# Kernel tuning notes

Measured on AMD Instinct MI355X. Metric: run time of the kernel, lower is better.

## Reference

```python
import jax, jax.numpy as jnp
import numpy as np

# Module config (init_kwargs): nodes = (64, 64)
NX, NY_NODES = 64, 64


def setup_inputs() -> dict:
    key = jax.random.key(0)
    data = jax.random.normal(key, (4, 3, 1024, 1024), dtype=jnp.float32)
    return {"data": data}


def reference(data):
    B, C, H, W = data.shape
    scale = W // NX                    # = 16
    ny = H // scale                    # grid rows (= 64 here)
    nx = NX
    N = nx * ny                        # num_nodes = 4096
    p = scale - 1                      # original slices x1:x2 with x2=x1+scale-1 -> (scale-1) pixels

    # [B, C, ny, p, nx, p] top-left (scale-1)x(scale-1) sub-patch of each grid cell
    patches = data.reshape(B, C, ny, scale, nx, scale)[:, :, :, :p, :, :p]

    # L1 affinity between vertically / horizontally adjacent patches
    dv = jnp.abs(patches[:, :, 1:] - patches[:, :, :-1]).sum(axis=(1, 3, 5))          # [B, ny-1, nx]
    dh = jnp.abs(patches[:, :, :, :, 1:] - patches[:, :, :, :, :-1]).sum(axis=(1, 3, 5))  # [B, ny, nx-1]

    node = jnp.arange(ny)[:, None] * nx + jnp.arange(nx)[None, :]  # node_id = x + y*nx

    A = jnp.zeros((B, N, N), dtype=data.dtype)
    # vertical edges: self<->up/down
    lo_v = node[1:, :].ravel()   # lower cell of each vertical pair
    hi_v = node[:-1, :].ravel()  # upper cell
    dv_f = dv.reshape(B, -1)
    A = A.at[:, lo_v, hi_v].set(dv_f)   # self -> up
    A = A.at[:, hi_v, lo_v].set(dv_f)   # self -> down
    # horizontal edges: self<->left/right
    le_h = node[:, :-1].ravel()
    ri_h = node[:, 1:].ravel()
    dh_f = dh.reshape(B, -1)
    A = A.at[:, le_h, ri_h].set(dh_f)   # self -> right
    A = A.at[:, ri_h, le_h].set(dh_f)   # self -> left

    return A, data
```

## Files before the change

### kernel.cpp

```cpp
#include <hip/hip_runtime.h>

#define BB 4
#define CC 3
#define HH 1024
#define WW 1024
#define NXG 64
#define NYG 64
#define SCALE 16
#define PP 15
#define NNODE 4096

static const long long A_ELEMS    = (long long)BB * NNODE * NNODE;
static const long long DATA_ELEMS = (long long)BB * CC * HH * WW;

#define NV_PER_B 4032
#define NH_PER_B 4032
#define NV_TOT   16128
#define NE_TOT   32256

#define COPY_BLOCKS 512
#define EDGE_BLOCKS 8064

__global__ __launch_bounds__(256) void edge_copy_scatter(const float* __restrict__ data,
                                                         float* __restrict__ out) {
    if (blockIdx.x < COPY_BLOCKS) {
        long long i = (long long)blockIdx.x * 256 + threadIdx.x;
        const long long stride = (long long)COPY_BLOCKS * 256;
        const float4* __restrict__ src = (const float4*)data;
        float4* __restrict__ dst = (float4*)(out + A_ELEMS);
        const long long nvec = DATA_ELEMS / 4;
        for (; i < nvec; i += stride) dst[i] = src[i];
        return;
    }

    const int wave = (blockIdx.x - COPY_BLOCKS) * 4 + (threadIdx.x >> 6);
    const int lane = threadIdx.x & 63;
    const int r = lane >> 2;
    const int q = lane & 3;

    int b, y, x, n_lo, n_hi;
    long long delta;
    if (wave < NV_TOT) {
        const int e = wave;
        b = e / NV_PER_B; const int rem = e - b * NV_PER_B;
        y = rem >> 6; x = rem & 63;
        delta = (long long)SCALE * WW;
        n_lo = y * NXG + x; n_hi = n_lo + NXG;
    } else {
        const int e = wave - NV_TOT;
        b = e / NH_PER_B; const int rem = e - b * NH_PER_B;
        y = rem / 63; x = rem - y * 63;
        delta = SCALE;
        n_lo = y * NXG + x; n_hi = n_lo + 1;
    }

    const float* p0 = data + (((long long)(b * CC)) * HH + (long long)y * SCALE + r) * WW
                           + x * SCALE + q * 4;
    float s = 0.f;
    if (r < PP) {
        #pragma unroll
        for (int c = 0; c < CC; ++c) {
            const float* p = p0 + (long long)c * HH * WW;
            const float4 a  = *(const float4*)p;
            const float4 nb = *(const float4*)(p + delta);
            float d = fabsf(nb.x - a.x) + fabsf(nb.y - a.y) + fabsf(nb.z - a.z);
            if (q != 3) d += fabsf(nb.w - a.w);
            s += d;
        }
    }
    #pragma unroll
    for (int off = 32; off; off >>= 1) s += __shfl_down(s, off, 64);

    if (lane == 0) {
        float* Ab = out + (long long)b * NNODE * NNODE;
        Ab[(long long)n_hi * NNODE + n_lo] = s;
        Ab[(long long)n_lo * NNODE + n_hi] = s;
    }
}

extern "C" void kernel_launch(void* const* d_in, const int* in_sizes, int n_in,
                              void* d_out, int out_size, void* d_ws, size_t ws_size,
                              hipStream_t stream) {
    const float* data = (const float*)d_in[0];
    float* out = (float*)d_out;

    hipMemsetAsync(out, 0, (size_t)A_ELEMS * sizeof(float), stream);

    edge_copy_scatter<<<COPY_BLOCKS + EDGE_BLOCKS, 256, 0, stream>>>(data, out);
}
```

Measured before the change: 355.3 us.

## Fuse zero-fill with edge scatter by writing full adjacency rows per node

Removes the separate memset of the 256 MB adjacency matrix. Each node now gets one block that computes its four neighbour affinities and writes its whole output row, zeros included, with nontemporal vector stores. The data copy also switches to nontemporal stores. Each edge affinity is now computed twice, once from each endpoint, and a block barrier is added. The total output written stays the same, but it now happens in a single kernel with one pass of stores.

```diff
diff --git a/kernel.cpp b/kernel.cpp
--- a/kernel.cpp
+++ b/kernel.cpp
@@ -5,64 +5,61 @@
 #define HH 1024
 #define WW 1024
 #define NXG 64
-#define NYG 64
 #define SCALE 16
 #define PP 15
 #define NNODE 4096
 
+typedef float floatx4 __attribute__((ext_vector_type(4)));
+
 static const long long A_ELEMS    = (long long)BB * NNODE * NNODE;
 static const long long DATA_ELEMS = (long long)BB * CC * HH * WW;
 
-#define NV_PER_B 4032
-#define NH_PER_B 4032
-#define NV_TOT   16128
-#define NE_TOT   32256
+#define COPY_BLOCKS 512
+#define ROW_BLOCKS  (BB * NNODE)
 
-#define COPY_BLOCKS 512
-#define EDGE_BLOCKS 8064
-
-__global__ __launch_bounds__(256) void edge_copy_scatter(const float* __restrict__ data,
-                                                         float* __restrict__ out) {
+__global__ __launch_bounds__(256) void fused_band_fill(const float* __restrict__ data,
+                                                       float* __restrict__ out) {
     if (blockIdx.x < COPY_BLOCKS) {
         long long i = (long long)blockIdx.x * 256 + threadIdx.x;
         const long long stride = (long long)COPY_BLOCKS * 256;
-        const float4* __restrict__ src = (const float4*)data;
-        float4* __restrict__ dst = (float4*)(out + A_ELEMS);
+        const floatx4* __restrict__ src = (const floatx4*)data;
+        floatx4* dst = (floatx4*)(out + A_ELEMS);
         const long long nvec = DATA_ELEMS / 4;
-        for (; i < nvec; i += stride) dst[i] = src[i];
+        for (; i < nvec; i += stride) {
+            floatx4 v = src[i];
+            __builtin_nontemporal_store(v, dst + i);
+        }
         return;
     }
 
-    const int wave = (blockIdx.x - COPY_BLOCKS) * 4 + (threadIdx.x >> 6);
+    const int rb = blockIdx.x - COPY_BLOCKS;
+    const int b  = rb >> 12;
+    const int n  = rb & (NNODE - 1);
+    const int y  = n >> 6;
+    const int x  = n & 63;
+
+    const int w    = threadIdx.x >> 6;
     const int lane = threadIdx.x & 63;
-    const int r = lane >> 2;
-    const int q = lane & 3;
+    const int r    = lane >> 2;
+    const int q    = lane & 3;
 
-    int b, y, x, n_lo, n_hi;
-    long long delta;
-    if (wave < NV_TOT) {
-        const int e = wave;
-        b = e / NV_PER_B; const int rem = e - b * NV_PER_B;
-        y = rem >> 6; x = rem & 63;
-        delta = (long long)SCALE * WW;
-        n_lo = y * NXG + x; n_hi = n_lo + NXG;
-    } else {
-        const int e = wave - NV_TOT;
-        b = e / NH_PER_B; const int rem = e - b * NH_PER_B;
-        y = rem / 63; x = rem - y * 63;
-        delta = SCALE;
-        n_lo = y * NXG + x; n_hi = n_lo + 1;
+    bool valid; int gy, gx; long long delta;
+    switch (w) {
+        case 0:  valid = (y > 0);  gy = y - 1; gx = x;     delta = (long long)SCALE * WW; break;
+        case 1:  valid = (y < 63); gy = y;     gx = x;     delta = (long long)SCALE * WW; break;
+        case 2:  valid = (x > 0);  gy = y;     gx = x - 1; delta = SCALE;                 break;
+        default: valid = (x < 63); gy = y;     gx = x;     delta = SCALE;                 break;
     }
 
-    const float* p0 = data + (((long long)(b * CC)) * HH + (long long)y * SCALE + r) * WW
-                           + x * SCALE + q * 4;
     float s = 0.f;
-    if (r < PP) {
+    if (valid && r < PP) {
+        const float* p0 = data + (((long long)(b * CC)) * HH + (long long)(gy * SCALE + r)) * WW
+                               + gx * SCALE + q * 4;
         #pragma unroll
         for (int c = 0; c < CC; ++c) {
             const float* p = p0 + (long long)c * HH * WW;
-            const float4 a  = *(const float4*)p;
-            const float4 nb = *(const float4*)(p + delta);
+            const floatx4 a  = *(const floatx4*)p;
+            const floatx4 nb = *(const floatx4*)(p + delta);
             float d = fabsf(nb.x - a.x) + fabsf(nb.y - a.y) + fabsf(nb.z - a.z);
             if (q != 3) d += fabsf(nb.w - a.w);
             s += d;
@@ -71,10 +68,27 @@
     #pragma unroll
     for (int off = 32; off; off >>= 1) s += __shfl_down(s, off, 64);
 
-    if (lane == 0) {
-        float* Ab = out + (long long)b * NNODE * NNODE;
-        Ab[(long long)n_hi * NNODE + n_lo] = s;
-        Ab[(long long)n_lo * NNODE + n_hi] = s;
+    __shared__ float ev[4];
+    if (lane == 0) ev[w] = s;
+    __syncthreads();
+
+    const float v_up = ev[0], v_dn = ev[1], v_lf = ev[2], v_rt = ev[3];
+    const int c_up = (y > 0)  ? n - NXG : -1;
+    const int c_dn = (y < 63) ? n + NXG : -1;
+    const int c_lf = (x > 0)  ? n - 1   : -1;
+    const int c_rt = (x < 63) ? n + 1   : -1;
+
+    float* rowp = out + ((long long)b * NNODE + n) * NNODE;
+    #pragma unroll
+    for (int k = 0; k < 4; ++k) {
+        const int cb = (int)(threadIdx.x + k * 256) << 2;
+        const int c0 = cb, c1 = cb + 1, c2 = cb + 2, c3 = cb + 3;
+        floatx4 v;
+        v.x = (c0 == c_up) ? v_up : (c0 == c_dn) ? v_dn : (c0 == c_lf) ? v_lf : (c0 == c_rt) ? v_rt : 0.f;
+        v.y = (c1 == c_up) ? v_up : (c1 == c_dn) ? v_dn : (c1 == c_lf) ? v_lf : (c1 == c_rt) ? v_rt : 0.f;
+        v.z = (c2 == c_up) ? v_up : (c2 == c_dn) ? v_dn : (c2 == c_lf) ? v_lf : (c2 == c_rt) ? v_rt : 0.f;
+        v.w = (c3 == c_up) ? v_up : (c3 == c_dn) ? v_dn : (c3 == c_lf) ? v_lf : (c3 == c_rt) ? v_rt : 0.f;
+        __builtin_nontemporal_store(v, (floatx4*)(rowp + cb));
     }
 }
 
@@ -83,8 +97,5 @@
                               hipStream_t stream) {
     const float* data = (const float*)d_in[0];
     float* out = (float*)d_out;
-
-    hipMemsetAsync(out, 0, (size_t)A_ELEMS * sizeof(float), stream);
-
-    edge_copy_scatter<<<COPY_BLOCKS + EDGE_BLOCKS, 256, 0, stream>>>(data, out);
+    fused_band_fill<<<COPY_BLOCKS + ROW_BLOCKS, 256, 0, stream>>>(data, out);
 }
```

Result: faster. 345.3 us (-2.8%).
